# Kernel tuning notes

Measured on AMD Instinct MI355X. Metric: run time of the kernel, lower is better.

## Reference

```python
import jax, jax.numpy as jnp
import numpy as np

D_MODEL = 1024
N_HEADS = 16
D_HEAD = 64
NEG = -1000000000.0


def setup_inputs() -> dict:
    key = jax.random.key(0)
    k1, k2, k3 = jax.random.split(key, 3)
    B, T = 2, 2048
    x = jax.random.normal(k1, (B, T, D_MODEL), dtype=jnp.float32)
    # qkv_proj: Linear(d_model, 3*H*D, bias=False) -> weight (3*H*D, d_model)
    w_qkv = jax.random.normal(k2, (3 * N_HEADS * D_HEAD, D_MODEL), dtype=jnp.float32) * (D_MODEL ** -0.5)
    # o_proj: Linear(H*D, d_model, bias=False) -> weight (d_model, H*D)
    w_o = jax.random.normal(k3, (D_MODEL, N_HEADS * D_HEAD), dtype=jnp.float32) * ((N_HEADS * D_HEAD) ** -0.5)
    return {"x": x, "w_qkv": w_qkv, "w_o": w_o}


def reference(x, w_qkv, w_o):
    B, T, _ = x.shape
    H, D = N_HEADS, D_HEAD
    scale = D ** -0.5
    qkv = jnp.einsum('btm,nm->btn', x, w_qkv).reshape(B, T, 3, H, D)
    q, k, v = qkv[:, :, 0], qkv[:, :, 1], qkv[:, :, 2]  # (B,T,H,D)
    # scores: (B,H,T,T)
    attn = jnp.einsum('bqhd,bkhd->bhqk', q, k) * scale
    causal = jnp.tril(jnp.ones((T, T), dtype=x.dtype))
    attn = attn + (1.0 - causal) * NEG
    attn = jax.nn.softmax(attn, axis=-1)
    out = jnp.einsum('bhqk,bkhd->bqhd', attn, v).reshape(B, T, H * D)
    out = jnp.einsum('btn,mn->btm', out, w_o)
    return (out, k, v)
```

## Files before the change

kernel.cpp:

```cpp
#include <hip/hip_runtime.h>
#include <cstdint>

typedef unsigned short u16;
typedef __bf16 bf16x8 __attribute__((ext_vector_type(8)));
typedef float f32x4 __attribute__((ext_vector_type(4)));
typedef short s4 __attribute__((ext_vector_type(4)));

#define T_SEQ 2048
#define NH 16

__device__ __forceinline__ u16 f2bf(float f) {
  union { float f; uint32_t u; } x; x.f = f;
  uint32_t r = (x.u + 0x7fffu + ((x.u >> 16) & 1u)) >> 16;
  return (u16)r;
}

__device__ __forceinline__ uint32_t pk2bf(float a, float b) {
  union { float f; uint32_t u; } x, y; x.f = a; y.f = b;
  uint32_t lo = (x.u + 0x7fffu + ((x.u >> 16) & 1u)) >> 16;
  uint32_t hi = (y.u + 0x7fffu + ((y.u >> 16) & 1u)) >> 16;
  return lo | (hi << 16);
}

__device__ __forceinline__ void cvt8(u16* dst, const float* src) {
  float4 a = *(const float4*)src;
  float4 b = *(const float4*)(src + 4);
  uint4 o;
  o.x = pk2bf(a.x, a.y); o.y = pk2bf(a.z, a.w);
  o.z = pk2bf(b.x, b.y); o.w = pk2bf(b.z, b.w);
  *(uint4*)dst = o;
}

__global__ __launch_bounds__(256) void cvt_all(const float* __restrict__ x,
                                               const float* __restrict__ wq,
                                               const float* __restrict__ wo,
                                               u16* __restrict__ dst) {
  int i = blockIdx.x * 256 + threadIdx.x;
  const float* src; int off;
  if (i < 524288)      { src = x;  off = 0; }
  else if (i < 917504) { src = wq; off = 524288; }
  else                 { src = wo; off = 917504; }
  cvt8(&dst[(size_t)i * 8], &src[(size_t)(i - off) * 8]);
}

__device__ __forceinline__ s4 cvt4(f32x4 v) {
  union { __bf16 b[4]; s4 s; } u;
  u.b[0] = (__bf16)v[0]; u.b[1] = (__bf16)v[1];
  u.b[2] = (__bf16)v[2]; u.b[3] = (__bf16)v[3];
  return u.s;
}

__device__ __forceinline__ f32x4 mfma16(s4 a, s4 b, f32x4 c) {
#if __has_builtin(__builtin_amdgcn_mfma_f32_16x16x16bf16_1k)
  return __builtin_amdgcn_mfma_f32_16x16x16bf16_1k(a, b, c, 0, 0, 0);
#else
  asm("v_mfma_f32_16x16x16_bf16 %0, %1, %2, %0" : "+v"(c) : "v"(a), "v"(b));
  return c;
#endif
}

__device__ __forceinline__ float exp2fast(float x) {
#if __has_builtin(__builtin_amdgcn_exp2f)
  return __builtin_amdgcn_exp2f(x);
#else
  float r; asm("v_exp_f32 %0, %1" : "=v"(r) : "v"(x)); return r;
#endif
}

__device__ __forceinline__ void gl_lds(const u16* g, u16* ldsbase) {
  __builtin_amdgcn_global_load_lds(
      (const __attribute__((address_space(1))) void*)g,
      (__attribute__((address_space(3))) void*)ldsbase, 16, 0, 0);
}

template <bool CF32, bool KV>
__global__ __launch_bounds__(256) void gemm_bt(
    const u16* __restrict__ A, const u16* __restrict__ W,
    void* __restrict__ Cp, float* __restrict__ outk, float* __restrict__ outv,
    int M, int N, int K) {
  __shared__ __align__(16) u16 As[128 * 64];
  __shared__ __align__(16) u16 Bs[128 * 64];
  const int tid  = threadIdx.x;
  const int bid  = blockIdx.y * gridDim.x + blockIdx.x;
  const int per  = (gridDim.x * gridDim.y) >> 3;
  const int swz  = (bid & 7) * per + (bid >> 3);
  const int n0   = (swz % gridDim.x) * 128;
  const int m0   = (swz / gridDim.x) * 128;
  const int lane = tid & 63;
  const int wave = tid >> 6;
  const int wm   = (wave >> 1) * 64;
  const int wn   = (wave & 1) * 64;
  const int l15  = lane & 15;
  const int quad = lane >> 4;
  const int srow = lane >> 3;
  const int sc   = lane & 7;

  f32x4 acc[4][4];
#pragma unroll
  for (int i = 0; i < 4; i++)
#pragma unroll
    for (int j = 0; j < 4; j++) acc[i][j] = (f32x4){0.f, 0.f, 0.f, 0.f};

  for (int k0 = 0; k0 < K; k0 += 64) {
    __syncthreads();
#pragma unroll
    for (int i = 0; i < 4; i++) {
      int r0  = (i * 4 + wave) * 8;
      int row = r0 + srow;
      int gc  = (sc ^ (row & 7)) << 3;
      gl_lds(&A[(size_t)(m0 + row) * K + k0 + gc], &As[r0 * 64]);
      gl_lds(&W[(size_t)(n0 + row) * K + k0 + gc], &Bs[r0 * 64]);
    }
    __syncthreads();
#pragma unroll
    for (int kk = 0; kk < 64; kk += 32) {
      bf16x8 af[4], bfr[4];
#pragma unroll
      for (int i = 0; i < 4; i++) {
        int arow = wm + i * 16 + l15;
        af[i] = *(const bf16x8*)((const char*)As + arow * 128 +
                                 ((((kk >> 3) + quad) ^ (arow & 7)) << 4));
      }
#pragma unroll
      for (int j = 0; j < 4; j++) {
        int brow = wn + j * 16 + l15;
        bfr[j] = *(const bf16x8*)((const char*)Bs + brow * 128 +
                                  ((((kk >> 3) + quad) ^ (brow & 7)) << 4));
      }
#pragma unroll
      for (int i = 0; i < 4; i++)
#pragma unroll
        for (int j = 0; j < 4; j++)
          acc[i][j] = __builtin_amdgcn_mfma_f32_16x16x32_bf16(af[i], bfr[j], acc[i][j], 0, 0, 0);
    }
  }
#pragma unroll
  for (int i = 0; i < 4; i++)
#pragma unroll
    for (int j = 0; j < 4; j++)
#pragma unroll
      for (int r = 0; r < 4; r++) {
        int row = m0 + wm + i * 16 + quad * 4 + r;
        int col = n0 + wn + j * 16 + l15;
        float v = acc[i][j][r];
        if constexpr (CF32) {
          ((float*)Cp)[(size_t)row * N + col] = v;
        } else {
          ((u16*)Cp)[(size_t)row * N + col] = f2bf(v);
          if constexpr (KV) {
            if (col >= 2048)      outv[(size_t)row * 1024 + (col - 2048)] = v;
            else if (col >= 1024) outk[(size_t)row * 1024 + (col - 1024)] = v;
          }
        }
      }
}

__global__ __launch_bounds__(256) void transpose_v(const u16* __restrict__ qkv,
                                                   u16* __restrict__ vt) {
  __shared__ __align__(16) u16 tile[64 * 72];
  int t0 = blockIdx.x * 64;
  int bh = blockIdx.y;
  int b = bh >> 4, h = bh & 15;
  int tid = threadIdx.x;
  int t8 = tid & 7, rowb = tid >> 3;
#pragma unroll
  for (int r = 0; r < 2; r++) {
    int row = rowb + r * 32;
    *(uint4*)&tile[row * 72 + t8 * 8] =
        *(const uint4*)&qkv[((size_t)b * T_SEQ + t0 + row) * 3072 + 2048 + h * 64 + t8 * 8];
  }
  __syncthreads();
#pragma unroll
  for (int r = 0; r < 2; r++) {
    int d = rowb + r * 32;
    union { u16 s[8]; uint4 u; } tmp;
#pragma unroll
    for (int e = 0; e < 8; e++) tmp.s[e] = tile[(t8 * 8 + e) * 72 + d];
    *(uint4*)&vt[((size_t)(b * NH + h) * 64 + d) * 2048 + t0 + t8 * 8] = tmp.u;
  }
}

__global__ __launch_bounds__(512) void attn(const u16* __restrict__ qkv,
                                            const u16* __restrict__ vt,
                                            u16* __restrict__ o) {
  __shared__ __align__(16) u16 Ks[2][64 * 64];
  __shared__ __align__(16) u16 Vts[2][64 * 64];

  const int tid  = threadIdx.x;
  const int p    = 15 - (int)blockIdx.x;
  const int bh   = blockIdx.y;
  const int b    = bh >> 4, h = bh & 15;
  const int lane = tid & 63, wave = tid >> 6;
  const int grp  = wave >> 2;
  const int w4   = wave & 3;
  const int l15  = lane & 15, quad = lane >> 4;
  const int srow = lane >> 3, sc = lane & 7;
  const size_t qbase = (size_t)b * T_SEQ * 3072;
  const size_t vbase = (size_t)(b * NH + h) * 64 * 2048;
  const float C = 0.1803368801f;

  const int qt   = 2 * p + 1 - grp;
  const int wq0  = qt * 64 + w4 * 16;
  const int qrow = wq0 + l15;

  const u16* qp = &qkv[qbase + (size_t)qrow * 3072 + h * 64];
  const bf16x8 qf0 = *(const bf16x8*)&qp[quad * 8];
  const bf16x8 qf1 = *(const bf16x8*)&qp[32 + quad * 8];

  f32x4 acc_o[4];
#pragma unroll
  for (int n = 0; n < 4; n++) acc_o[n] = (f32x4){0.f, 0.f, 0.f, 0.f};
  float m2run = -1e30f, lrun = 0.f;

  auto stage = [&](int d, int k0) {
    int r0  = wave * 8;
    int row = r0 + srow;
    int gc  = (sc ^ (row & 7)) << 3;
    gl_lds(&qkv[qbase + (size_t)(k0 + row) * 3072 + 1024 + h * 64 + gc], &Ks[d][r0 * 64]);
    gl_lds(&vt[vbase + (size_t)row * 2048 + k0 + gc], &Vts[d][r0 * 64]);
  };

  stage(0, 0);

  const int steps = 2 * p + 2;
  for (int s = 0; s < steps; s++) {
    const int d = s & 1;
    __syncthreads();

    if (s + 1 < steps) stage(d ^ 1, (s + 1) * 64);

    if (s <= qt) {
      const int k0 = s * 64;

      f32x4 sacc[4];
#pragma unroll
      for (int j = 0; j < 4; j++) sacc[j] = (f32x4){0.f, 0.f, 0.f, 0.f};
#pragma unroll
      for (int j = 0; j < 4; j++) {
        int krow = j * 16 + l15;
        const char* kb = (const char*)&Ks[d][0] + krow * 128;
        bf16x8 kfa = *(const bf16x8*)(kb + ((quad ^ (krow & 7)) << 4));
        bf16x8 kfb = *(const bf16x8*)(kb + (((4 + quad) ^ (krow & 7)) << 4));
        sacc[j] = __builtin_amdgcn_mfma_f32_16x16x32_bf16(kfa, qf0, sacc[j], 0, 0, 0);
        sacc[j] = __builtin_amdgcn_mfma_f32_16x16x32_bf16(kfb, qf1, sacc[j], 0, 0, 0);
      }

      if (s == qt) {
#pragma unroll
        for (int j = 0; j < 4; j++)
#pragma unroll
          for (int r = 0; r < 4; r++) {
            int k = k0 + j * 16 + quad * 4 + r;
            if (k > qrow) sacc[j][r] = -1e30f;
          }
      }

      float mj[4];
#pragma unroll
      for (int j = 0; j < 4; j++)
        mj[j] = fmaxf(fmaxf(sacc[j][0], sacc[j][1]), fmaxf(sacc[j][2], sacc[j][3]));
      float mx = fmaxf(fmaxf(mj[0], mj[1]), fmaxf(mj[2], mj[3]));
      mx = fmaxf(mx, __shfl_xor(mx, 16));
      mx = fmaxf(mx, __shfl_xor(mx, 32));
      const float m2x = mx * C;

      if (!__all(m2x <= m2run + 8.0f)) {
        const float m2new = fmaxf(m2run, m2x);
        const float alpha = exp2fast(m2run - m2new);
        lrun *= alpha;
        m2run = m2new;
#pragma unroll
        for (int r = 0; r < 4; r++) {
          float ar = __shfl(alpha, quad * 4 + r);
#pragma unroll
          for (int n = 0; n < 4; n++) acc_o[n][r] *= ar;
        }
      }

      const float nm = m2run;
      float ts[4];
#pragma unroll
      for (int j = 0; j < 4; j++) {
#pragma unroll
        for (int r = 0; r < 4; r++) sacc[j][r] = exp2fast(fmaf(sacc[j][r], C, -nm));
        ts[j] = (sacc[j][0] + sacc[j][1]) + (sacc[j][2] + sacc[j][3]);
      }
      float sum = (ts[0] + ts[1]) + (ts[2] + ts[3]);
      sum += __shfl_xor(sum, 16);
      sum += __shfl_xor(sum, 32);
      lrun += sum;

      s4 pa[4];
#pragma unroll
      for (int j = 0; j < 4; j++) pa[j] = cvt4(sacc[j]);

#pragma unroll
      for (int j = 0; j < 4; j++)
#pragma unroll
        for (int n = 0; n < 4; n++) {
          int vrow = n * 16 + l15;
          int ch = (j * 2 + (quad >> 1)) ^ (vrow & 7);
          const s4 vf = *(const s4*)((const char*)&Vts[d][0] + vrow * 128 +
                                     (ch << 4) + ((quad & 1) << 3));
          acc_o[n] = mfma16(pa[j], vf, acc_o[n]);
        }
    }
  }

  const float linv = 1.0f / lrun;
#pragma unroll
  for (int r = 0; r < 4; r++) {
    const float lr = __shfl(linv, quad * 4 + r);
    const int row = wq0 + quad * 4 + r;
#pragma unroll
    for (int n = 0; n < 4; n++)
      o[(size_t)(b * T_SEQ + row) * 1024 + h * 64 + n * 16 + l15] =
          f2bf(acc_o[n][r] * lr);
  }
}

extern "C" void kernel_launch(void* const* d_in, const int* in_sizes, int n_in,
                              void* d_out, int out_size, void* d_ws, size_t ws_size,
                              hipStream_t stream) {
  const float* x     = (const float*)d_in[0];
  const float* w_qkv = (const float*)d_in[1];
  const float* w_o   = (const float*)d_in[2];
  float* out  = (float*)d_out;
  float* outk = out + (size_t)4194304;
  float* outv = out + (size_t)8388608;

  u16* qkv = (u16*)d_ws;
  u16* vt  = qkv + (size_t)4096 * 3072;
  u16* ao  = vt  + (size_t)4194304;
  u16* xb  = ao  + (size_t)4194304;
  u16* wqb = xb  + (size_t)4194304;
  u16* wob = wqb + (size_t)3145728;

  cvt_all<<<4096, 256, 0, stream>>>(x, w_qkv, w_o, xb);

  gemm_bt<false, true><<<dim3(24, 32), 256, 0, stream>>>(
      xb, wqb, qkv, outk, outv, 4096, 3072, 1024);
  transpose_v<<<dim3(32, 32), 256, 0, stream>>>(qkv, vt);
  attn<<<dim3(16, 32), 512, 0, stream>>>(qkv, vt, ao);
  gemm_bt<true, false><<<dim3(8, 32), 256, 0, stream>>>(
      ao, wob, out, nullptr, nullptr, 4096, 1024, 1024);
}
```

Measured before the change: 226.0 us.

## Pair causal q-tiles per attention block with triple-buffered KV pipeline; 8-wave output GEMM

```diff
diff --git a/kernel.cpp b/kernel.cpp
--- a/kernel.cpp
+++ b/kernel.cpp
@@ -73,11 +73,13 @@
       (__attribute__((address_space(3))) void*)ldsbase, 16, 0, 0);
 }
 
-template <bool CF32, bool KV>
-__global__ __launch_bounds__(256) void gemm_bt(
+template <bool CF32, bool KV, int WAVES>
+__global__ __launch_bounds__(WAVES * 64) void gemm_bt(
     const u16* __restrict__ A, const u16* __restrict__ W,
     void* __restrict__ Cp, float* __restrict__ outk, float* __restrict__ outv,
     int M, int N, int K) {
+  constexpr int NJ = (WAVES == 4) ? 4 : 2;
+  constexpr int SI = 16 / WAVES;
   __shared__ __align__(16) u16 As[128 * 64];
   __shared__ __align__(16) u16 Bs[128 * 64];
   const int tid  = threadIdx.x;
@@ -88,24 +90,24 @@
   const int m0   = (swz / gridDim.x) * 128;
   const int lane = tid & 63;
   const int wave = tid >> 6;
-  const int wm   = (wave >> 1) * 64;
-  const int wn   = (wave & 1) * 64;
+  const int wm   = (WAVES == 4 ? (wave >> 1) : (wave >> 2)) * 64;
+  const int wn   = (WAVES == 4 ? (wave & 1) * 64 : (wave & 3) * 32);
   const int l15  = lane & 15;
   const int quad = lane >> 4;
   const int srow = lane >> 3;
   const int sc   = lane & 7;
 
-  f32x4 acc[4][4];
+  f32x4 acc[4][NJ];
 #pragma unroll
   for (int i = 0; i < 4; i++)
 #pragma unroll
-    for (int j = 0; j < 4; j++) acc[i][j] = (f32x4){0.f, 0.f, 0.f, 0.f};
+    for (int j = 0; j < NJ; j++) acc[i][j] = (f32x4){0.f, 0.f, 0.f, 0.f};
 
   for (int k0 = 0; k0 < K; k0 += 64) {
     __syncthreads();
 #pragma unroll
-    for (int i = 0; i < 4; i++) {
-      int r0  = (i * 4 + wave) * 8;
+    for (int i = 0; i < SI; i++) {
+      int r0  = (i * WAVES + wave) * 8;
       int row = r0 + srow;
       int gc  = (sc ^ (row & 7)) << 3;
       gl_lds(&A[(size_t)(m0 + row) * K + k0 + gc], &As[r0 * 64]);
@@ -114,7 +116,7 @@
     __syncthreads();
 #pragma unroll
     for (int kk = 0; kk < 64; kk += 32) {
-      bf16x8 af[4], bfr[4];
+      bf16x8 af[4], bfr[NJ];
 #pragma unroll
       for (int i = 0; i < 4; i++) {
         int arow = wm + i * 16 + l15;
@@ -122,7 +124,7 @@
                                  ((((kk >> 3) + quad) ^ (arow & 7)) << 4));
       }
 #pragma unroll
-      for (int j = 0; j < 4; j++) {
+      for (int j = 0; j < NJ; j++) {
         int brow = wn + j * 16 + l15;
         bfr[j] = *(const bf16x8*)((const char*)Bs + brow * 128 +
                                   ((((kk >> 3) + quad) ^ (brow & 7)) << 4));
@@ -130,14 +132,14 @@
 #pragma unroll
       for (int i = 0; i < 4; i++)
 #pragma unroll
-        for (int j = 0; j < 4; j++)
+        for (int j = 0; j < NJ; j++)
           acc[i][j] = __builtin_amdgcn_mfma_f32_16x16x32_bf16(af[i], bfr[j], acc[i][j], 0, 0, 0);
     }
   }
 #pragma unroll
   for (int i = 0; i < 4; i++)
 #pragma unroll
-    for (int j = 0; j < 4; j++)
+    for (int j = 0; j < NJ; j++)
 #pragma unroll
       for (int r = 0; r < 4; r++) {
         int row = m0 + wm + i * 16 + quad * 4 + r;
@@ -180,143 +182,167 @@
   }
 }
 
-__global__ __launch_bounds__(512) void attn(const u16* __restrict__ qkv,
+__global__ __launch_bounds__(256) void attn(const u16* __restrict__ qkv,
                                             const u16* __restrict__ vt,
                                             u16* __restrict__ o) {
-  __shared__ __align__(16) u16 Ks[2][64 * 64];
-  __shared__ __align__(16) u16 Vts[2][64 * 64];
+  __shared__ __align__(16) u16 Ks[3][64 * 64];
+  __shared__ __align__(16) u16 Vts[3][64 * 64];
 
   const int tid  = threadIdx.x;
-  const int p    = 15 - (int)blockIdx.x;
+  const int pair = blockIdx.x;
   const int bh   = blockIdx.y;
   const int b    = bh >> 4, h = bh & 15;
   const int lane = tid & 63, wave = tid >> 6;
-  const int grp  = wave >> 2;
-  const int w4   = wave & 3;
   const int l15  = lane & 15, quad = lane >> 4;
   const int srow = lane >> 3, sc = lane & 7;
   const size_t qbase = (size_t)b * T_SEQ * 3072;
   const size_t vbase = (size_t)(b * NH + h) * 64 * 2048;
   const float C = 0.1803368801f;
 
-  const int qt   = 2 * p + 1 - grp;
-  const int wq0  = qt * 64 + w4 * 16;
-  const int qrow = wq0 + l15;
-
-  const u16* qp = &qkv[qbase + (size_t)qrow * 3072 + h * 64];
-  const bf16x8 qf0 = *(const bf16x8*)&qp[quad * 8];
-  const bf16x8 qf1 = *(const bf16x8*)&qp[32 + quad * 8];
+  const int qtA = pair, qtB = 31 - pair;
+  const int wq0A = qtA * 64 + wave * 16;
+  const int wq0B = qtB * 64 + wave * 16;
+  const u16* qpA = &qkv[qbase + (size_t)(wq0A + l15) * 3072 + h * 64];
+  const u16* qpB = &qkv[qbase + (size_t)(wq0B + l15) * 3072 + h * 64];
+  bf16x8 qf0 = *(const bf16x8*)&qpA[quad * 8];
+  bf16x8 qf1 = *(const bf16x8*)&qpA[32 + quad * 8];
+  const bf16x8 qB0 = *(const bf16x8*)&qpB[quad * 8];
+  const bf16x8 qB1 = *(const bf16x8*)&qpB[32 + quad * 8];
+
+  int qt = qtA, wq0 = wq0A, qrow = wq0A + l15;
 
   f32x4 acc_o[4];
 #pragma unroll
   for (int n = 0; n < 4; n++) acc_o[n] = (f32x4){0.f, 0.f, 0.f, 0.f};
   float m2run = -1e30f, lrun = 0.f;
 
-  auto stage = [&](int d, int k0) {
-    int r0  = wave * 8;
-    int row = r0 + srow;
-    int gc  = (sc ^ (row & 7)) << 3;
-    gl_lds(&qkv[qbase + (size_t)(k0 + row) * 3072 + 1024 + h * 64 + gc], &Ks[d][r0 * 64]);
-    gl_lds(&vt[vbase + (size_t)row * 2048 + k0 + gc], &Vts[d][r0 * 64]);
+  auto ktof = [&](int s) { return (s > pair) ? (s - pair - 1) : s; };
+
+  auto stage = [&](int buf, int s) {
+    const int k0 = ktof(s) * 64;
+#pragma unroll
+    for (int i = 0; i < 2; i++) {
+      int r0  = (wave * 2 + i) * 8;
+      int row = r0 + srow;
+      int gc  = (sc ^ (row & 7)) << 3;
+      gl_lds(&qkv[qbase + (size_t)(k0 + row) * 3072 + 1024 + h * 64 + gc], &Ks[buf][r0 * 64]);
+      gl_lds(&vt[vbase + (size_t)row * 2048 + k0 + gc], &Vts[buf][r0 * 64]);
+    }
   };
 
+  auto writeout = [&]() {
+    float linv = 1.0f / lrun;
+#pragma unroll
+    for (int r = 0; r < 4; r++) {
+      float lr = __shfl(linv, quad * 4 + r);
+      int row = wq0 + quad * 4 + r;
+#pragma unroll
+      for (int n = 0; n < 4; n++)
+        o[(size_t)(b * T_SEQ + row) * 1024 + h * 64 + n * 16 + l15] =
+            f2bf(acc_o[n][r] * lr);
+    }
+  };
+
   stage(0, 0);
-
-  const int steps = 2 * p + 2;
+  stage(1, 1);
+
+  const int steps = 33;
   for (int s = 0; s < steps; s++) {
-    const int d = s & 1;
-    __syncthreads();
-
-    if (s + 1 < steps) stage(d ^ 1, (s + 1) * 64);
-
-    if (s <= qt) {
-      const int k0 = s * 64;
-
-      f32x4 sacc[4];
-#pragma unroll
-      for (int j = 0; j < 4; j++) sacc[j] = (f32x4){0.f, 0.f, 0.f, 0.f};
-#pragma unroll
-      for (int j = 0; j < 4; j++) {
-        int krow = j * 16 + l15;
-        const char* kb = (const char*)&Ks[d][0] + krow * 128;
-        bf16x8 kfa = *(const bf16x8*)(kb + ((quad ^ (krow & 7)) << 4));
-        bf16x8 kfb = *(const bf16x8*)(kb + (((4 + quad) ^ (krow & 7)) << 4));
-        sacc[j] = __builtin_amdgcn_mfma_f32_16x16x32_bf16(kfa, qf0, sacc[j], 0, 0, 0);
-        sacc[j] = __builtin_amdgcn_mfma_f32_16x16x32_bf16(kfb, qf1, sacc[j], 0, 0, 0);
-      }
-
-      if (s == qt) {
-#pragma unroll
-        for (int j = 0; j < 4; j++)
-#pragma unroll
-          for (int r = 0; r < 4; r++) {
-            int k = k0 + j * 16 + quad * 4 + r;
-            if (k > qrow) sacc[j][r] = -1e30f;
-          }
-      }
-
-      float mj[4];
+    if (s < steps - 1) asm volatile("s_waitcnt vmcnt(4)" ::: "memory");
+    else               asm volatile("s_waitcnt vmcnt(0)" ::: "memory");
+    __builtin_amdgcn_s_barrier();
+    __builtin_amdgcn_sched_barrier(0);
+
+    if (s + 2 < steps) stage((s + 2) % 3, s + 2);
+
+    if (s == pair + 1) {
+      writeout();
+#pragma unroll
+      for (int n = 0; n < 4; n++) acc_o[n] = (f32x4){0.f, 0.f, 0.f, 0.f};
+      m2run = -1e30f; lrun = 0.f;
+      qt = qtB; wq0 = wq0B; qrow = wq0B + l15;
+      qf0 = qB0; qf1 = qB1;
+    }
+
+    const int cur = s % 3;
+    const int kt  = ktof(s);
+    const int k0  = kt * 64;
+
+    f32x4 sacc[4];
+#pragma unroll
+    for (int j = 0; j < 4; j++) sacc[j] = (f32x4){0.f, 0.f, 0.f, 0.f};
+#pragma unroll
+    for (int j = 0; j < 4; j++) {
+      int krow = j * 16 + l15;
+      const char* kb = (const char*)&Ks[cur][0] + krow * 128;
+      bf16x8 kfa = *(const bf16x8*)(kb + ((quad ^ (krow & 7)) << 4));
+      bf16x8 kfb = *(const bf16x8*)(kb + (((4 + quad) ^ (krow & 7)) << 4));
+      sacc[j] = __builtin_amdgcn_mfma_f32_16x16x32_bf16(kfa, qf0, sacc[j], 0, 0, 0);
+      sacc[j] = __builtin_amdgcn_mfma_f32_16x16x32_bf16(kfb, qf1, sacc[j], 0, 0, 0);
+    }
+
+    if (kt == qt) {
 #pragma unroll
       for (int j = 0; j < 4; j++)
-        mj[j] = fmaxf(fmaxf(sacc[j][0], sacc[j][1]), fmaxf(sacc[j][2], sacc[j][3]));
-      float mx = fmaxf(fmaxf(mj[0], mj[1]), fmaxf(mj[2], mj[3]));
-      mx = fmaxf(mx, __shfl_xor(mx, 16));
-      mx = fmaxf(mx, __shfl_xor(mx, 32));
-      const float m2x = mx * C;
-
-      if (!__all(m2x <= m2run + 8.0f)) {
-        const float m2new = fmaxf(m2run, m2x);
-        const float alpha = exp2fast(m2run - m2new);
-        lrun *= alpha;
-        m2run = m2new;
 #pragma unroll
         for (int r = 0; r < 4; r++) {
-          float ar = __shfl(alpha, quad * 4 + r);
-#pragma unroll
-          for (int n = 0; n < 4; n++) acc_o[n][r] *= ar;
+          int k = k0 + j * 16 + quad * 4 + r;
+          if (k > qrow) sacc[j][r] = -1e30f;
         }
-      }
-
-      const float nm = m2run;
-      float ts[4];
-#pragma unroll
-      for (int j = 0; j < 4; j++) {
-#pragma unroll
-        for (int r = 0; r < 4; r++) sacc[j][r] = exp2fast(fmaf(sacc[j][r], C, -nm));
-        ts[j] = (sacc[j][0] + sacc[j][1]) + (sacc[j][2] + sacc[j][3]);
-      }
-      float sum = (ts[0] + ts[1]) + (ts[2] + ts[3]);
-      sum += __shfl_xor(sum, 16);
-      sum += __shfl_xor(sum, 32);
-      lrun += sum;
-
-      s4 pa[4];
-#pragma unroll
-      for (int j = 0; j < 4; j++) pa[j] = cvt4(sacc[j]);
-
-#pragma unroll
-      for (int j = 0; j < 4; j++)
-#pragma unroll
-        for (int n = 0; n < 4; n++) {
-          int vrow = n * 16 + l15;
-          int ch = (j * 2 + (quad >> 1)) ^ (vrow & 7);
-          const s4 vf = *(const s4*)((const char*)&Vts[d][0] + vrow * 128 +
-                                     (ch << 4) + ((quad & 1) << 3));
-          acc_o[n] = mfma16(pa[j], vf, acc_o[n]);
-        }
-    }
+    }
+
+    float mj[4];
+#pragma unroll
+    for (int j = 0; j < 4; j++)
+      mj[j] = fmaxf(fmaxf(sacc[j][0], sacc[j][1]), fmaxf(sacc[j][2], sacc[j][3]));
+    float mx = fmaxf(fmaxf(mj[0], mj[1]), fmaxf(mj[2], mj[3]));
+    mx = fmaxf(mx, __shfl_xor(mx, 16));
+    mx = fmaxf(mx, __shfl_xor(mx, 32));
+    const float m2x = mx * C;
+
+    if (!__all(m2x <= m2run + 8.0f)) {
+      const float m2new = fmaxf(m2run, m2x);
+      const float alpha = exp2fast(m2run - m2new);
+      lrun *= alpha;
+      m2run = m2new;
+#pragma unroll
+      for (int r = 0; r < 4; r++) {
+        float ar = __shfl(alpha, quad * 4 + r);
+#pragma unroll
+        for (int n = 0; n < 4; n++) acc_o[n][r] *= ar;
+      }
+    }
+
+    const float nm = m2run;
+    float ts[4];
+#pragma unroll
+    for (int j = 0; j < 4; j++) {
+#pragma unroll
+      for (int r = 0; r < 4; r++) sacc[j][r] = exp2fast(fmaf(sacc[j][r], C, -nm));
+      ts[j] = (sacc[j][0] + sacc[j][1]) + (sacc[j][2] + sacc[j][3]);
+    }
+    float sum = (ts[0] + ts[1]) + (ts[2] + ts[3]);
+    sum += __shfl_xor(sum, 16);
+    sum += __shfl_xor(sum, 32);
+    lrun += sum;
+
+    s4 pa[4];
+#pragma unroll
+    for (int j = 0; j < 4; j++) pa[j] = cvt4(sacc[j]);
+
+#pragma unroll
+    for (int j = 0; j < 4; j++)
+#pragma unroll
+      for (int n = 0; n < 4; n++) {
+        int vrow = n * 16 + l15;
+        int ch = (j * 2 + (quad >> 1)) ^ (vrow & 7);
+        const s4 vf = *(const s4*)((const char*)&Vts[cur][0] + vrow * 128 +
+                                   (ch << 4) + ((quad & 1) << 3));
+        acc_o[n] = mfma16(pa[j], vf, acc_o[n]);
+      }
   }
 
-  const float linv = 1.0f / lrun;
-#pragma unroll
-  for (int r = 0; r < 4; r++) {
-    const float lr = __shfl(linv, quad * 4 + r);
-    const int row = wq0 + quad * 4 + r;
-#pragma unroll
-    for (int n = 0; n < 4; n++)
-      o[(size_t)(b * T_SEQ + row) * 1024 + h * 64 + n * 16 + l15] =
-          f2bf(acc_o[n][r] * lr);
-  }
+  writeout();
 }
 
 extern "C" void kernel_launch(void* const* d_in, const int* in_sizes, int n_in,
@@ -338,10 +364,10 @@
 
   cvt_all<<<4096, 256, 0, stream>>>(x, w_qkv, w_o, xb);
 
-  gemm_bt<false, true><<<dim3(24, 32), 256, 0, stream>>>(
+  gemm_bt<false, true, 4><<<dim3(24, 32), 256, 0, stream>>>(
       xb, wqb, qkv, outk, outv, 4096, 3072, 1024);
   transpose_v<<<dim3(32, 32), 256, 0, stream>>>(qkv, vt);
-  attn<<<dim3(16, 32), 512, 0, stream>>>(qkv, vt, ao);
-  gemm_bt<true, false><<<dim3(8, 32), 256, 0, stream>>>(
+  attn<<<dim3(16, 32), 256, 0, stream>>>(qkv, vt, ao);
+  gemm_bt<true, false, 8><<<dim3(8, 32), 512, 0, stream>>>(
       ao, wob, out, nullptr, nullptr, 4096, 1024, 1024);
 }
```

Result: faster. 211.0 us (-6.6%).
